# Performance work log

Measured on AMD Instinct MI355X. Metric: run time of the kernel, lower is better.

The kernel has to match this reference:

```python
import jax, jax.numpy as jnp
import numpy as np

N = 50000
E = 1600000
D_IN = 512
EPS = 1e-5


def setup_inputs() -> dict:
    key = jax.random.key(0)
    ks = jax.random.split(key, 20)
    p = lambda k, shape: jax.random.normal(k, shape, dtype=jnp.float32) * 0.05
    return {
        "x": jax.random.normal(ks[0], (N, D_IN), dtype=jnp.float32),
        "edge_index": jax.random.randint(ks[1], (2, E), 0, N),
        "edge_weight": jax.random.uniform(ks[2], (E,), dtype=jnp.float32),
        # conv1: ChebConv(512->400) with K=1,2,3 (weight per Chebyshev order)
        "W1a": p(ks[3], (1, D_IN, 400)), "b1a": p(ks[4], (400,)),
        "W1b": p(ks[5], (2, D_IN, 400)), "b1b": p(ks[6], (400,)),
        "W1c": p(ks[7], (3, D_IN, 400)), "b1c": p(ks[8], (400,)),
        "g1": jnp.ones((1200,), jnp.float32), "beta1": jnp.zeros((1200,), jnp.float32),
        # conv2: ChebConv(1200->100) with K=1,2,3
        "W2a": p(ks[9], (1, 1200, 100)), "b2a": p(ks[10], (100,)),
        "W2b": p(ks[11], (2, 1200, 100)), "b2b": p(ks[12], (100,)),
        "W2c": p(ks[13], (3, 1200, 100)), "b2c": p(ks[14], (100,)),
        "g2": jnp.ones((300,), jnp.float32), "beta2": jnp.zeros((300,), jnp.float32),
        "Wl": p(ks[15], (300, 10)), "bl": p(ks[16], (10,)),
    }


def _cheb(x, row, col, norm, W, b):
    """PyG ChebConv forward: out = sum_k T_k(L_hat) x @ W[k] + b.
    L_hat (sym norm, lambda_max=2) = -D^{-1/2} A D^{-1/2}, zero diagonal,
    applied as scatter: (L_hat h)[col] += norm_e * h[row]."""
    K = W.shape[0]
    n = x.shape[0]
    prop = lambda h: jax.ops.segment_sum(norm[:, None] * h[row], col, num_segments=n)
    out = x @ W[0]
    Tx_prev, Tx = x, None
    if K >= 2:
        Tx = prop(x)
        out = out + Tx @ W[1]
    for k in range(2, K):
        Tx_new = 2.0 * prop(Tx) - Tx_prev
        out = out + Tx_new @ W[k]
        Tx_prev, Tx = Tx, Tx_new
    return out + b


def _bn(h, g, beta):
    # BatchNorm over nodes (training-mode batch statistics, biased var)
    mu = h.mean(axis=0)
    var = h.var(axis=0)
    return (h - mu) * jax.lax.rsqrt(var + EPS) * g + beta


def reference(x, edge_index, edge_weight, W1a, b1a, W1b, b1b, W1c, b1c, g1, beta1,
              W2a, b2a, W2b, b2b, W2c, b2c, g2, beta2, Wl, bl):
    row, col = edge_index[0], edge_index[1]
    deg = jax.ops.segment_sum(edge_weight, row, num_segments=x.shape[0])
    safe = jnp.where(deg > 0, deg, 1.0)
    dis = jnp.where(deg > 0, jax.lax.rsqrt(safe), 0.0)  # deg^{-1/2}, inf -> 0
    norm = -dis[row] * edge_weight * dis[col]  # scaled-Laplacian edge weights

    h = jnp.concatenate([
        _cheb(x, row, col, norm, W1a, b1a),
        _cheb(x, row, col, norm, W1b, b1b),
        _cheb(x, row, col, norm, W1c, b1c)], axis=1)  # [N, 1200]
    h = jax.nn.relu(_bn(h, g1, beta1))

    h = jnp.concatenate([
        _cheb(h, row, col, norm, W2a, b2a),
        _cheb(h, row, col, norm, W2b, b2b),
        _cheb(h, row, col, norm, W2c, b2c)], axis=1)  # [N, 300]
    h = _bn(h, g2, beta2)

    logits = h @ Wl + bl  # [N, 10]
    return jax.nn.log_softmax(logits, axis=1)
```

## Files before the change

### kernel.cpp

```cpp
#include <hip/hip_runtime.h>
#include <math.h>

#define EPSB 1e-5f

typedef __attribute__((ext_vector_type(8))) short short8;
typedef __attribute__((ext_vector_type(4))) float floatx4;
typedef __attribute__((ext_vector_type(2))) float floatx2;

__device__ inline float bf2f(unsigned short h) {
  union { unsigned int u; float f; } v; v.u = ((unsigned int)h) << 16; return v.f;
}
__device__ inline unsigned short f2bf(float f) {
  union { float f; unsigned int u; } v; v.f = f;
  unsigned int r = v.u + 0x7fffu + ((v.u >> 16) & 1u);
  return (unsigned short)(r >> 16);
}

__device__ __forceinline__ void gl2lds16(const unsigned short* g, unsigned short* l) {
  __builtin_amdgcn_global_load_lds(
      (const __attribute__((address_space(1))) unsigned int*)g,
      (__attribute__((address_space(3))) unsigned int*)l, 16, 0, 0);
}

__device__ __forceinline__ void pk4(floatx2* a, uint4 g, floatx2 wv) {
  unsigned int u[4] = {g.x, g.y, g.z, g.w};
#pragma unroll
  for (int j = 0; j < 4; j++) {
    union { unsigned int q; float f; } lo, hi;
    lo.q = u[j] << 16;
    hi.q = u[j] & 0xffff0000u;
    floatx2 v; v[0] = lo.f; v[1] = hi.f;
    asm("v_pk_fma_f32 %0, %1, %2, %0" : "+v"(a[j]) : "v"(v), "v"(wv));
  }
}


__global__ void degcnt_kernel(const int* __restrict__ row, const int* __restrict__ col,
                              const float* __restrict__ ew,
                              float* __restrict__ deg, int* __restrict__ cnt, int E) {
  int e = blockIdx.x * blockDim.x + threadIdx.x;
  if (e < E) {
    atomicAdd(&deg[row[e]], ew[e]);
    atomicAdd(&cnt[col[e]], 1);
  }
}

__global__ void dis_kernel(float* deg, int n) {
  int i = blockIdx.x * blockDim.x + threadIdx.x;
  if (i < n) { float d = deg[i]; deg[i] = d > 0.f ? rsqrtf(d) : 0.f; }
}

__global__ __launch_bounds__(1024) void scan1_kernel(const int* __restrict__ cnt,
                                                     int* __restrict__ off,
                                                     int* __restrict__ bsum, int n) {
  __shared__ int buf[1024];
  int tid = threadIdx.x;
  int idx = blockIdx.x * 1024 + tid;
  int v = (idx < n) ? cnt[idx] : 0;
  buf[tid] = v;
  __syncthreads();
  for (int s = 1; s < 1024; s <<= 1) {
    int t = (tid >= s) ? buf[tid - s] : 0;
    __syncthreads();
    if (tid >= s) buf[tid] += t;
    __syncthreads();
  }
  if (idx < n) off[idx] = buf[tid] - v;
  if (tid == 1023) bsum[blockIdx.x] = buf[1023];
}

__global__ void scan2_kernel(int* __restrict__ bsum, int* __restrict__ off,
                             int nb, int n) {
  if (threadIdx.x == 0 && blockIdx.x == 0) {
    int run = 0;
    for (int k = 0; k < nb; k++) { int t = bsum[k]; bsum[k] = run; run += t; }
    off[n] = run;
  }
}

__global__ void scan3_kernel(int* __restrict__ off, const int* __restrict__ bsum, int n) {
  int i = blockIdx.x * blockDim.x + threadIdx.x;
  if (i < n) off[i] += bsum[i >> 10];
}

__global__ void copy_kernel(const int* __restrict__ src, int* __restrict__ dst, int n) {
  int i = blockIdx.x * blockDim.x + threadIdx.x;
  if (i < n) dst[i] = src[i];
}

__global__ void fill_kernel(const int* __restrict__ row, const int* __restrict__ col,
                            const float* __restrict__ ew, const float* __restrict__ dis,
                            int* __restrict__ wptr,
                            int2* __restrict__ ePack, int2* __restrict__ eA,
                            int2* __restrict__ eZ, int2* __restrict__ eU, int E) {
  int e = blockIdx.x * blockDim.x + threadIdx.x;
  if (e < E) {
    int r = row[e], c = col[e];
    int p = atomicAdd(&wptr[c], 1);
    float nv = -dis[r] * ew[e] * dis[c];
    int wb = __float_as_int(nv);
    ePack[p] = make_int2(r, wb);
    eA[p] = make_int2(r * 3072, wb);
    eZ[p] = make_int2(r * 608, wb);
    eU[p] = make_int2(r * 208, wb);
  }
}


__global__ void cast_x_kernel(const float* __restrict__ x, unsigned short* __restrict__ xb,
                              int N) {
  int idx = blockIdx.x * blockDim.x + threadIdx.x;
  if (idx >= N * 128) return;
  int row = idx >> 7, c4 = idx & 127;
  float4 v = *reinterpret_cast<const float4*>(x + (size_t)row * 512 + c4 * 4);
  union { unsigned int u[2]; } p;
  p.u[0] = (unsigned int)f2bf(v.x) | ((unsigned int)f2bf(v.y) << 16);
  p.u[1] = (unsigned int)f2bf(v.z) | ((unsigned int)f2bf(v.w) << 16);
  *reinterpret_cast<uint2*>(xb + (size_t)row * 1536 + c4 * 4) = make_uint2(p.u[0], p.u[1]);
}

__global__ void wprep_kernel(const float* __restrict__ W, unsigned short* __restrict__ Bt,
                             int Ktot, int Nout, int ldBt, int rowOff) {
  int idx = blockIdx.x * blockDim.x + threadIdx.x;
  if (idx >= Ktot * Nout) return;
  int k = idx / Nout, n = idx - k * Nout;
  Bt[(size_t)(rowOff + n) * ldBt + k] = f2bf(W[idx]);
}

__global__ void padzero_kernel(unsigned short* __restrict__ h, int N) {
  int i = blockIdx.x * blockDim.x + threadIdx.x;
  if (i >= N * 2) return;
  *reinterpret_cast<uint4*>(h + (size_t)(i >> 1) * 1216 + 1200 + (i & 1) * 8) =
      make_uint4(0, 0, 0, 0);
}

__global__ void bcat_kernel(const float* __restrict__ a, const float* __restrict__ b,
                            const float* __restrict__ c, float* __restrict__ dst) {
  int i = threadIdx.x;
  if (i < 100) dst[i] = a[i];
  else if (i < 200) dst[i] = b[i - 100];
  else if (i < 300) dst[i] = c[i - 200];
}

__global__ __launch_bounds__(256) void prop_chunk_kernel(
    unsigned short* __restrict__ base, int ld,
    int srcCol, int dstCol, int subCol,
    const int* __restrict__ off, const int2* __restrict__ eA,
    float scale, int N) {
  int chunk = blockIdx.x & 7;
  int g = blockIdx.x >> 3;
  int tid = threadIdx.x;
  int c8 = tid & 7;
  int v = g * 32 + (tid >> 3);
  bool valid = v < N;
  int vv = valid ? v : N - 1;
  int co = chunk * 64 + c8 * 8;
  const char* src = (const char*)(base + srcCol + co);
  int s = off[vv], e = off[vv + 1];
  floatx2 a2[4] = {}, b2[4] = {};
  int i = s;
  for (; i + 3 < e; i += 4) {
    int2 p0 = eA[i];
    int2 p1 = eA[i + 1];
    int2 p2 = eA[i + 2];
    int2 p3 = eA[i + 3];
    uint4 g0 = *reinterpret_cast<const uint4*>(src + (unsigned)p0.x);
    uint4 g1 = *reinterpret_cast<const uint4*>(src + (unsigned)p1.x);
    uint4 g2 = *reinterpret_cast<const uint4*>(src + (unsigned)p2.x);
    uint4 g3 = *reinterpret_cast<const uint4*>(src + (unsigned)p3.x);
    floatx2 w0; w0[0] = w0[1] = __int_as_float(p0.y);
    floatx2 w1; w1[0] = w1[1] = __int_as_float(p1.y);
    floatx2 w2; w2[0] = w2[1] = __int_as_float(p2.y);
    floatx2 w3; w3[0] = w3[1] = __int_as_float(p3.y);
    pk4(a2, g0, w0);
    pk4(b2, g1, w1);
    pk4(a2, g2, w2);
    pk4(b2, g3, w3);
  }
  for (; i < e; i++) {
    int2 p = eA[i];
    uint4 gg = *reinterpret_cast<const uint4*>(src + (unsigned)p.x);
    floatx2 wv; wv[0] = wv[1] = __int_as_float(p.y);
    pk4(a2, gg, wv);
  }
  if (!valid) return;
  float a[8];
#pragma unroll
  for (int j = 0; j < 4; j++) {
    a[2 * j]     = a2[j][0] + b2[j][0];
    a[2 * j + 1] = a2[j][1] + b2[j][1];
  }
  if (subCol >= 0) {
    uint4 sv = *reinterpret_cast<const uint4*>(base + subCol + co + (size_t)v * ld);
    a[0] = scale * a[0] - bf2f((unsigned short)(sv.x & 0xffff));
    a[1] = scale * a[1] - bf2f((unsigned short)(sv.x >> 16));
    a[2] = scale * a[2] - bf2f((unsigned short)(sv.y & 0xffff));
    a[3] = scale * a[3] - bf2f((unsigned short)(sv.y >> 16));
    a[4] = scale * a[4] - bf2f((unsigned short)(sv.z & 0xffff));
    a[5] = scale * a[5] - bf2f((unsigned short)(sv.z >> 16));
    a[6] = scale * a[6] - bf2f((unsigned short)(sv.w & 0xffff));
    a[7] = scale * a[7] - bf2f((unsigned short)(sv.w >> 16));
  }
  uint4 o;
  o.x = (unsigned int)f2bf(a[0]) | ((unsigned int)f2bf(a[1]) << 16);
  o.y = (unsigned int)f2bf(a[2]) | ((unsigned int)f2bf(a[3]) << 16);
  o.z = (unsigned int)f2bf(a[4]) | ((unsigned int)f2bf(a[5]) << 16);
  o.w = (unsigned int)f2bf(a[6]) | ((unsigned int)f2bf(a[7]) << 16);
  *reinterpret_cast<uint4*>(base + dstCol + co + (size_t)v * ld) = o;
}

__global__ void prop_z_kernel(const unsigned short* __restrict__ Zcat,
                              const int* __restrict__ off, const int2* __restrict__ eZ,
                              float* __restrict__ h2f, unsigned short* __restrict__ U1) {
  int v = blockIdx.x;
  int f8 = threadIdx.x;
  if (f8 >= 38) return;
  int s = off[v], e = off[v + 1];
  const char* srcB = (const char*)Zcat + f8 * 16;
  floatx2 a2[4] = {}, b2[4] = {};
  int i = s;
  for (; i + 3 < e; i += 4) {
    int2 p0 = eZ[i];
    int2 p1 = eZ[i + 1];
    int2 p2 = eZ[i + 2];
    int2 p3 = eZ[i + 3];
    uint4 g0 = *reinterpret_cast<const uint4*>(srcB + (unsigned)p0.x);
    uint4 g1 = *reinterpret_cast<const uint4*>(srcB + (unsigned)p1.x);
    uint4 g2 = *reinterpret_cast<const uint4*>(srcB + (unsigned)p2.x);
    uint4 g3 = *reinterpret_cast<const uint4*>(srcB + (unsigned)p3.x);
    floatx2 w0; w0[0] = w0[1] = __int_as_float(p0.y);
    floatx2 w1; w1[0] = w1[1] = __int_as_float(p1.y);
    floatx2 w2; w2[0] = w2[1] = __int_as_float(p2.y);
    floatx2 w3; w3[0] = w3[1] = __int_as_float(p3.y);
    pk4(a2, g0, w0);
    pk4(b2, g1, w1);
    pk4(a2, g2, w2);
    pk4(b2, g3, w3);
  }
  for (; i < e; i++) {
    int2 p = eZ[i];
    uint4 raw = *reinterpret_cast<const uint4*>(srcB + (unsigned)p.x);
    floatx2 wv; wv[0] = wv[1] = __int_as_float(p.y);
    pk4(a2, raw, wv);
  }
  float a[8];
#pragma unroll
  for (int j = 0; j < 4; j++) {
    a[2 * j]     = a2[j][0] + b2[j][0];
    a[2 * j + 1] = a2[j][1] + b2[j][1];
  }
  if (f8 < 25) {
    float* p = h2f + (size_t)v * 300 + 100 + f8 * 8;
#pragma unroll
    for (int j = 0; j < 8; j++) p[j] += a[j];
  } else {
    uint4 o;
    o.x = (unsigned int)f2bf(a[0]) | ((unsigned int)f2bf(a[1]) << 16);
    o.y = (unsigned int)f2bf(a[2]) | ((unsigned int)f2bf(a[3]) << 16);
    o.z = (unsigned int)f2bf(a[4]) | ((unsigned int)f2bf(a[5]) << 16);
    o.w = (unsigned int)f2bf(a[6]) | ((unsigned int)f2bf(a[7]) << 16);
    *reinterpret_cast<uint4*>(U1 + (size_t)v * 104 + (f8 - 25) * 8) = o;
  }
}

__global__ void prop_u_kernel(const unsigned short* __restrict__ U1,
                              const int* __restrict__ off, const int2* __restrict__ eU,
                              const unsigned short* __restrict__ Zcat,
                              float* __restrict__ h2f) {
  int v = blockIdx.x;
  int f8 = threadIdx.x;
  if (f8 >= 13) return;
  int s = off[v], e = off[v + 1];
  const char* srcB = (const char*)U1 + f8 * 16;
  floatx2 a2[4] = {}, b2[4] = {};
  int i = s;
  for (; i + 3 < e; i += 4) {
    int2 p0 = eU[i];
    int2 p1 = eU[i + 1];
    int2 p2 = eU[i + 2];
    int2 p3 = eU[i + 3];
    uint4 g0 = *reinterpret_cast<const uint4*>(srcB + (unsigned)p0.x);
    uint4 g1 = *reinterpret_cast<const uint4*>(srcB + (unsigned)p1.x);
    uint4 g2 = *reinterpret_cast<const uint4*>(srcB + (unsigned)p2.x);
    uint4 g3 = *reinterpret_cast<const uint4*>(srcB + (unsigned)p3.x);
    floatx2 w0; w0[0] = w0[1] = __int_as_float(p0.y);
    floatx2 w1; w1[0] = w1[1] = __int_as_float(p1.y);
    floatx2 w2; w2[0] = w2[1] = __int_as_float(p2.y);
    floatx2 w3; w3[0] = w3[1] = __int_as_float(p3.y);
    pk4(a2, g0, w0);
    pk4(b2, g1, w1);
    pk4(a2, g2, w2);
    pk4(b2, g3, w3);
  }
  for (; i < e; i++) {
    int2 p = eU[i];
    uint4 raw = *reinterpret_cast<const uint4*>(srcB + (unsigned)p.x);
    floatx2 wv; wv[0] = wv[1] = __int_as_float(p.y);
    pk4(a2, raw, wv);
  }
  float a[8];
#pragma unroll
  for (int j = 0; j < 4; j++) {
    a[2 * j]     = a2[j][0] + b2[j][0];
    a[2 * j + 1] = a2[j][1] + b2[j][1];
  }
  const unsigned short* z2 = Zcat + (size_t)v * 304 + 200;
  float* p = h2f + (size_t)v * 300 + 200;
#pragma unroll
  for (int j = 0; j < 8; j++) {
    int c = f8 * 8 + j;
    if (c < 100) p[c] += 2.f * a[j] - bf2f(z2[c]);
  }
}

__global__ __launch_bounds__(256) void gemm_bf16_kernel(
    const unsigned short* __restrict__ A, int lda,
    const unsigned short* __restrict__ Bt, int ldb,
    int M, int Nc, int K,
    const float* __restrict__ bias,
    unsigned short* __restrict__ Cb, float* __restrict__ Cf, int ldc, int c0,
    int accumulate) {
  __shared__ __align__(16) unsigned short As[128 * 32];
  __shared__ __align__(16) unsigned short Bs[128 * 32];
  int tid = threadIdx.x;
  int wave = tid >> 6, lane = tid & 63;
  int q = lane >> 4, mn = lane & 15;
  int wr = wave >> 1, wc = wave & 1;
  int row0 = blockIdx.y * 128, col0 = blockIdx.x * 128;
  floatx4 acc[4][4] = {};

  const unsigned short* ga[2];
  const unsigned short* gb[2];
  unsigned short* la[2];
  unsigned short* lb[2];
#pragma unroll
  for (int j = 0; j < 2; j++) {
    int c = j * 256 + tid;
    int r = c >> 2, cw = (c & 3) * 8;
    int gr = row0 + r; if (gr > M - 1) gr = M - 1;
    ga[j] = A + (size_t)gr * lda + cw;
    int gn = col0 + r; if (gn > Nc - 1) gn = Nc - 1;
    gb[j] = Bt + (size_t)gn * ldb + cw;
    la[j] = &As[(j * 256 + wave * 64) * 8];
    lb[j] = &Bs[(j * 256 + wave * 64) * 8];
  }

  for (int k0 = 0; k0 < K; k0 += 32) {
#pragma unroll
    for (int j = 0; j < 2; j++) {
      gl2lds16(ga[j] + k0, la[j]);
      gl2lds16(gb[j] + k0, lb[j]);
    }
    __syncthreads();

    short8 af[4], bf[4];
#pragma unroll
    for (int i = 0; i < 4; i++) {
      af[i] = *reinterpret_cast<const short8*>(&As[(wr * 64 + i * 16 + mn) * 32 + q * 8]);
      bf[i] = *reinterpret_cast<const short8*>(&Bs[(wc * 64 + i * 16 + mn) * 32 + q * 8]);
    }
#pragma unroll
    for (int mi = 0; mi < 4; mi++)
#pragma unroll
      for (int ni = 0; ni < 4; ni++)
        acc[mi][ni] = __builtin_amdgcn_mfma_f32_16x16x32_bf16(af[mi], bf[ni], acc[mi][ni], 0, 0, 0);
    __syncthreads();
  }

#pragma unroll
  for (int mi = 0; mi < 4; mi++) {
#pragma unroll
    for (int ni = 0; ni < 4; ni++) {
      int gcol = col0 + wc * 64 + ni * 16 + mn;
      if (gcol >= Nc) continue;
      float b = bias ? bias[gcol] : 0.f;
#pragma unroll
      for (int r = 0; r < 4; r++) {
        int grow = row0 + wr * 64 + mi * 16 + q * 4 + r;
        if (grow >= M) continue;
        float v = acc[mi][ni][r] + b;
        if (Cb) {
          Cb[(size_t)grow * ldc + c0 + gcol] = f2bf(v);
        } else {
          float* p = Cf + (size_t)grow * ldc + c0 + gcol;
          if (accumulate) v += *p;
          *p = v;
        }
      }
    }
  }
}

__global__ void bn_stats_bf16_kernel(const unsigned short* __restrict__ h, int ld, int C,
                                     int N, float* __restrict__ sums) {
  int c = blockIdx.x * blockDim.x + threadIdx.x;
  if (c >= C) return;
  int r0 = blockIdx.y * 256;
  int r1 = min(N, r0 + 256);
  float s = 0.f, s2 = 0.f;
  for (int r = r0; r < r1; r++) {
    float v = bf2f(h[(size_t)r * ld + c]);
    s += v; s2 += v * v;
  }
  atomicAdd(&sums[c], s);
  atomicAdd(&sums[C + c], s2);
}

__global__ void scsh_kernel(const float* __restrict__ sums, const float* __restrict__ g,
                            const float* __restrict__ beta, float invN, int C,
                            float* __restrict__ scSh) {
  int c = blockIdx.x * blockDim.x + threadIdx.x;
  if (c >= C) return;
  float mu = sums[c] * invN;
  float var = sums[C + c] * invN - mu * mu;
  float s = rsqrtf(var + EPSB) * g[c];
  scSh[c] = s;
  scSh[C + c] = beta[c] - mu * s;
}

__global__ void bn_apply_bf16_kernel(unsigned short* __restrict__ h, int ld, int C8, int N,
                                     const float* __restrict__ scSh, int Cfull, int relu) {
  int idx = blockIdx.x * blockDim.x + threadIdx.x;
  if (idx >= N * C8) return;
  int row = idx / C8, c8 = idx - row * C8;
  unsigned short* p = h + (size_t)row * ld + c8 * 8;
  uint4 raw = *reinterpret_cast<uint4*>(p);
  float v[8];
  v[0] = bf2f((unsigned short)(raw.x & 0xffff)); v[1] = bf2f((unsigned short)(raw.x >> 16));
  v[2] = bf2f((unsigned short)(raw.y & 0xffff)); v[3] = bf2f((unsigned short)(raw.y >> 16));
  v[4] = bf2f((unsigned short)(raw.z & 0xffff)); v[5] = bf2f((unsigned short)(raw.z >> 16));
  v[6] = bf2f((unsigned short)(raw.w & 0xffff)); v[7] = bf2f((unsigned short)(raw.w >> 16));
#pragma unroll
  for (int j = 0; j < 8; j++) {
    int c = c8 * 8 + j;
    float o = v[j] * scSh[c] + scSh[Cfull + c];
    if (relu) o = fmaxf(o, 0.f);
    v[j] = o;
  }
  uint4 o;
  o.x = (unsigned int)f2bf(v[0]) | ((unsigned int)f2bf(v[1]) << 16);
  o.y = (unsigned int)f2bf(v[2]) | ((unsigned int)f2bf(v[3]) << 16);
  o.z = (unsigned int)f2bf(v[4]) | ((unsigned int)f2bf(v[5]) << 16);
  o.w = (unsigned int)f2bf(v[6]) | ((unsigned int)f2bf(v[7]) << 16);
  *reinterpret_cast<uint4*>(p) = o;
}

__global__ void bn_stats_kernel(const float* __restrict__ h, int C, int N,
                                float* __restrict__ sums) {
  int c = blockIdx.x * blockDim.x + threadIdx.x;
  if (c >= C) return;
  int r0 = blockIdx.y * 256;
  int r1 = min(N, r0 + 256);
  float s = 0.f, s2 = 0.f;
  for (int r = r0; r < r1; r++) {
    float v = h[(size_t)r * C + c];
    s += v; s2 += v * v;
  }
  atomicAdd(&sums[c], s);
  atomicAdd(&sums[C + c], s2);
}

__global__ void bn_apply_kernel(float* __restrict__ h, int C, int N,
                                const float* __restrict__ sums, const float* __restrict__ g,
                                const float* __restrict__ beta, float invN, int relu) {
  int C4 = C >> 2;
  int c4 = blockIdx.x * blockDim.x + threadIdx.x;
  if (c4 >= C4) return;
  float sc[4], sh[4];
#pragma unroll
  for (int j = 0; j < 4; j++) {
    int c = c4 * 4 + j;
    float mu = sums[c] * invN;
    float var = sums[C + c] * invN - mu * mu;
    float s = rsqrtf(var + EPSB) * g[c];
    sc[j] = s; sh[j] = beta[c] - mu * s;
  }
  int r0 = blockIdx.y * 256, r1 = min(N, r0 + 256);
  for (int r = r0; r < r1; r++) {
    float4* p = reinterpret_cast<float4*>(h + (size_t)r * C) + c4;
    float4 v = *p;
    v.x = v.x * sc[0] + sh[0]; v.y = v.y * sc[1] + sh[1];
    v.z = v.z * sc[2] + sh[2]; v.w = v.w * sc[3] + sh[3];
    if (relu) {
      v.x = fmaxf(v.x, 0.f); v.y = fmaxf(v.y, 0.f);
      v.z = fmaxf(v.z, 0.f); v.w = fmaxf(v.w, 0.f);
    }
    *p = v;
  }
}


__global__ __launch_bounds__(256) void final_bn_kernel(const float* __restrict__ h2,
                                                       const float* __restrict__ scSh,
                                                       const float* __restrict__ Wl,
                                                       const float* __restrict__ bl,
                                                       float* __restrict__ out, int N) {
  __shared__ float Ws[3000];
  __shared__ float S[600];
  for (int i = threadIdx.x; i < 3000; i += 256) Ws[i] = Wl[i];
  for (int i = threadIdx.x; i < 600; i += 256) S[i] = scSh[i];
  __syncthreads();
  int r = blockIdx.x * blockDim.x + threadIdx.x;
  if (r >= N) return;
  float acc[10];
#pragma unroll
  for (int c = 0; c < 10; c++) acc[c] = bl[c];
  const float* hr = h2 + (size_t)r * 300;
  for (int k = 0; k < 300; k++) {
    float x = hr[k] * S[k] + S[300 + k];
#pragma unroll
    for (int c = 0; c < 10; c++) acc[c] += x * Ws[k * 10 + c];
  }
  float mx = acc[0];
#pragma unroll
  for (int c = 1; c < 10; c++) mx = fmaxf(mx, acc[c]);
  float se = 0.f;
#pragma unroll
  for (int c = 0; c < 10; c++) se += expf(acc[c] - mx);
  float lz = mx + logf(se);
#pragma unroll
  for (int c = 0; c < 10; c++) out[(size_t)r * 10 + c] = acc[c] - lz;
}

__global__ __launch_bounds__(256) void final_kernel(const float* __restrict__ h2,
                                                    const float* __restrict__ Wl,
                                                    const float* __restrict__ bl,
                                                    float* __restrict__ out, int N) {
  __shared__ float Ws[3000];
  for (int i = threadIdx.x; i < 3000; i += 256) Ws[i] = Wl[i];
  __syncthreads();
  int r = blockIdx.x * blockDim.x + threadIdx.x;
  if (r >= N) return;
  float acc[10];
#pragma unroll
  for (int c = 0; c < 10; c++) acc[c] = bl[c];
  const float* hr = h2 + (size_t)r * 300;
  for (int k = 0; k < 300; k++) {
    float x = hr[k];
#pragma unroll
    for (int c = 0; c < 10; c++) acc[c] += x * Ws[k * 10 + c];
  }
  float mx = acc[0];
#pragma unroll
  for (int c = 1; c < 10; c++) mx = fmaxf(mx, acc[c]);
  float se = 0.f;
#pragma unroll
  for (int c = 0; c < 10; c++) se += expf(acc[c] - mx);
  float lz = mx + logf(se);
#pragma unroll
  for (int c = 0; c < 10; c++) out[(size_t)r * 10 + c] = acc[c] - lz;
}


__global__ void prop_kernel(const float* __restrict__ src, int srcLd4, int D4,
                            const int* __restrict__ off, const int2* __restrict__ ePack,
                            float* __restrict__ dst, int dstLd4,
                            const float* __restrict__ sub, int subLd4, float scale) {
  int v = blockIdx.x;
  int f4 = threadIdx.x;
  if (f4 >= D4) return;
  int s = off[v], e = off[v + 1];
  float ax = 0.f, ay = 0.f, az = 0.f, aw = 0.f;
  for (int i = s; i < e; i++) {
    int2 p = ePack[i];
    float w = __int_as_float(p.y);
    const float4 hv = *reinterpret_cast<const float4*>(src + ((size_t)p.x * srcLd4 + f4) * 4);
    ax += w * hv.x; ay += w * hv.y; az += w * hv.z; aw += w * hv.w;
  }
  float4 o;
  if (sub) {
    const float4 sv = *reinterpret_cast<const float4*>(sub + ((size_t)v * subLd4 + f4) * 4);
    o.x = scale * ax - sv.x; o.y = scale * ay - sv.y;
    o.z = scale * az - sv.z; o.w = scale * aw - sv.w;
  } else {
    o.x = ax; o.y = ay; o.z = az; o.w = aw;
  }
  *reinterpret_cast<float4*>(dst + ((size_t)v * dstLd4 + f4) * 4) = o;
}

#define BM 64
#define BN 64
#define BK 16

__global__ __launch_bounds__(256) void gemm_kernel(
    const float* __restrict__ A, int lda,
    const float* __restrict__ B, int ldb,
    float* __restrict__ C, int ldc, int c0,
    int M, int Nc, int K,
    const float* __restrict__ bias, int accumulate) {
  __shared__ float As[BK][BM + 4];
  __shared__ float Bs[BK][BN + 4];
  int tid = threadIdx.x;
  int tx = tid & 15, ty = tid >> 4;
  int row0 = blockIdx.y * BM, col0 = blockIdx.x * BN;
  float acc[4][4] = {};
  int aM = tid >> 2;
  int aK = (tid & 3) << 2;
  int bK = tid >> 4;
  int bN = (tid & 15) << 2;
  for (int k0 = 0; k0 < K; k0 += BK) {
    float4 av = make_float4(0.f, 0.f, 0.f, 0.f);
    int ar = row0 + aM;
    if (ar < M && k0 + aK < K)
      av = *reinterpret_cast<const float4*>(A + (size_t)ar * lda + k0 + aK);
    As[aK + 0][aM] = av.x; As[aK + 1][aM] = av.y;
    As[aK + 2][aM] = av.z; As[aK + 3][aM] = av.w;
    float4 bv = make_float4(0.f, 0.f, 0.f, 0.f);
    int bc = col0 + bN;
    if (bc < Nc && k0 + bK < K)
      bv = *reinterpret_cast<const float4*>(B + (size_t)(k0 + bK) * ldb + bc);
    Bs[bK][bN + 0] = bv.x; Bs[bK][bN + 1] = bv.y;
    Bs[bK][bN + 2] = bv.z; Bs[bK][bN + 3] = bv.w;
    __syncthreads();
#pragma unroll
    for (int k = 0; k < BK; k++) {
      float a0 = As[k][ty * 4 + 0], a1 = As[k][ty * 4 + 1];
      float a2 = As[k][ty * 4 + 2], a3 = As[k][ty * 4 + 3];
      float b0 = Bs[k][tx * 4 + 0], b1 = Bs[k][tx * 4 + 1];
      float b2 = Bs[k][tx * 4 + 2], b3 = Bs[k][tx * 4 + 3];
      acc[0][0] += a0 * b0; acc[0][1] += a0 * b1; acc[0][2] += a0 * b2; acc[0][3] += a0 * b3;
      acc[1][0] += a1 * b0; acc[1][1] += a1 * b1; acc[1][2] += a1 * b2; acc[1][3] += a1 * b3;
      acc[2][0] += a2 * b0; acc[2][1] += a2 * b1; acc[2][2] += a2 * b2; acc[2][3] += a2 * b3;
      acc[3][0] += a3 * b0; acc[3][1] += a3 * b1; acc[3][2] += a3 * b2; acc[3][3] += a3 * b3;
    }
    __syncthreads();
  }
#pragma unroll
  for (int i = 0; i < 4; i++) {
    int r = row0 + ty * 4 + i;
    if (r >= M) continue;
#pragma unroll
    for (int j = 0; j < 4; j++) {
      int c = col0 + tx * 4 + j;
      if (c >= Nc) continue;
      float v = acc[i][j];
      if (bias) v += bias[c];
      float* p = C + (size_t)r * ldc + c0 + c;
      if (accumulate) *p += v; else *p = v;
    }
  }
}


extern "C" void kernel_launch(void* const* d_in, const int* in_sizes, int n_in,
                              void* d_out, int out_size, void* d_ws, size_t ws_size,
                              hipStream_t stream) {
  const float* x   = (const float*)d_in[0];
  const int*   ei  = (const int*)d_in[1];
  const float* ew  = (const float*)d_in[2];
  const float* W1a = (const float*)d_in[3];
  const float* b1a = (const float*)d_in[4];
  const float* W1b = (const float*)d_in[5];
  const float* b1b = (const float*)d_in[6];
  const float* W1c = (const float*)d_in[7];
  const float* b1c = (const float*)d_in[8];
  const float* g1  = (const float*)d_in[9];
  const float* be1 = (const float*)d_in[10];
  const float* W2a = (const float*)d_in[11];
  const float* b2a = (const float*)d_in[12];
  const float* W2b = (const float*)d_in[13];
  const float* b2b = (const float*)d_in[14];
  const float* W2c = (const float*)d_in[15];
  const float* b2c = (const float*)d_in[16];
  const float* g2  = (const float*)d_in[17];
  const float* be2 = (const float*)d_in[18];
  const float* Wl  = (const float*)d_in[19];
  const float* bl  = (const float*)d_in[20];
  float* out = (float*)d_out;

  const int N = in_sizes[0] / 512;
  const int E = in_sizes[1] / 2;
  const int* row = ei;
  const int* col = ei + E;
  (void)n_in; (void)out_size;

  int eb = (E + 255) / 256;
  int nb = (N + 255) / 256;
  int nb1 = (N + 1023) / 1024;

  char* ws = (char*)d_ws;
  size_t o = 0;
  int2*  ePack = (int2*)(ws + o);  o += (size_t)E * 8;
  int2*  eA    = (int2*)(ws + o);  o += (size_t)E * 8;
  int2*  eZ    = (int2*)(ws + o);  o += (size_t)E * 8;
  int2*  eU    = (int2*)(ws + o);  o += (size_t)E * 8;
  float* dis   = (float*)(ws + o); o += (size_t)N * 4;
  int*   cnt   = (int*)(ws + o);   o += (size_t)N * 4;
  int*   off   = (int*)(ws + o);   o += (size_t)(N + 4) * 4;
  int*   wptr  = (int*)(ws + o);   o += (size_t)N * 4;
  int*   bsum  = (int*)(ws + o);   o += (size_t)(nb1 + 4) * 4;
  float* sums  = (float*)(ws + o); o += 2400 * 4;
  float* scSh  = (float*)(ws + o); o += 2400 * 4;
  float* bcat  = (float*)(ws + o); o += 304 * 4;
  o = (o + 255) & ~(size_t)255;
  size_t oCommon = o;

  size_t oA = oCommon;
  unsigned short* Bt1a = (unsigned short*)(ws + oA); oA += (size_t)400 * 512 * 2;
  unsigned short* Bt1b = (unsigned short*)(ws + oA); oA += (size_t)400 * 1024 * 2;
  unsigned short* Bt1c = (unsigned short*)(ws + oA); oA += (size_t)400 * 1536 * 2;
  unsigned short* Bt2cat0 = (unsigned short*)(ws + oA); oA += (size_t)304 * 1216 * 2;
  unsigned short* Bt2z    = (unsigned short*)(ws + oA); oA += (size_t)304 * 1216 * 2;
  oA = (oA + 255) & ~(size_t)255;
  unsigned short* h1n = (unsigned short*)(ws + oA); oA += (size_t)N * 1216 * 2;
  oA = (oA + 255) & ~(size_t)255;
  float* h2f = (float*)(ws + oA); oA += (size_t)N * 300 * 4;
  oA = (oA + 255) & ~(size_t)255;
  unsigned short* Xcat = (unsigned short*)(ws + oA); oA += (size_t)N * 1536 * 2;
  unsigned short* Zcat = Xcat;
  unsigned short* U1 = Xcat + (size_t)N * 304;

  bool planA = (ws_size >= oA);

  hipMemsetAsync(dis, 0, (size_t)N * 4, stream);
  hipMemsetAsync(cnt, 0, (size_t)N * 4, stream);
  degcnt_kernel<<<eb, 256, 0, stream>>>(row, col, ew, dis, cnt, E);
  dis_kernel<<<nb, 256, 0, stream>>>(dis, N);
  scan1_kernel<<<nb1, 1024, 0, stream>>>(cnt, off, bsum, N);
  scan2_kernel<<<1, 64, 0, stream>>>(bsum, off, nb1, N);
  scan3_kernel<<<nb, 256, 0, stream>>>(off, bsum, N);
  copy_kernel<<<nb, 256, 0, stream>>>(off, wptr, N);
  fill_kernel<<<eb, 256, 0, stream>>>(row, col, ew, dis, wptr, ePack, eA, eZ, eU, E);

  if (planA) {
    wprep_kernel<<<(400 * 512 + 255) / 256, 256, 0, stream>>>(W1a, Bt1a, 512, 400, 512, 0);
    wprep_kernel<<<(400 * 1024 + 255) / 256, 256, 0, stream>>>(W1b, Bt1b, 1024, 400, 1024, 0);
    wprep_kernel<<<(400 * 1536 + 255) / 256, 256, 0, stream>>>(W1c, Bt1c, 1536, 400, 1536, 0);
    hipMemsetAsync(Bt2cat0, 0, (size_t)304 * 1216 * 2, stream);
    hipMemsetAsync(Bt2z, 0, (size_t)304 * 1216 * 2, stream);
    wprep_kernel<<<(100 * 1200 + 255) / 256, 256, 0, stream>>>(W2a, Bt2cat0, 1200, 100, 1216, 0);
    wprep_kernel<<<(100 * 1200 + 255) / 256, 256, 0, stream>>>(W2b, Bt2cat0, 1200, 100, 1216, 100);
    wprep_kernel<<<(100 * 1200 + 255) / 256, 256, 0, stream>>>(W2c, Bt2cat0, 1200, 100, 1216, 200);
    wprep_kernel<<<(100 * 1200 + 255) / 256, 256, 0, stream>>>(W2b + 1200 * 100, Bt2z, 1200, 100, 1216, 0);
    wprep_kernel<<<(100 * 1200 + 255) / 256, 256, 0, stream>>>(W2c + 1200 * 100, Bt2z, 1200, 100, 1216, 100);
    wprep_kernel<<<(100 * 1200 + 255) / 256, 256, 0, stream>>>(W2c + 2 * 1200 * 100, Bt2z, 1200, 100, 1216, 200);
    bcat_kernel<<<1, 320, 0, stream>>>(b2a, b2b, b2c, bcat);
    cast_x_kernel<<<(N * 128 + 255) / 256, 256, 0, stream>>>(x, Xcat, N);
    padzero_kernel<<<(N * 2 + 255) / 256, 256, 0, stream>>>(h1n, N);

    int gridP = ((N + 31) / 32) * 8;
    prop_chunk_kernel<<<gridP, 256, 0, stream>>>(Xcat, 1536, 0, 512, -1,
                                                 off, eA, 1.f, N);
    prop_chunk_kernel<<<gridP, 256, 0, stream>>>(Xcat, 1536, 512, 1024, 0,
                                                 off, eA, 2.f, N);

    dim3 gA((400 + 127) / 128, (N + 127) / 128);
    gemm_bf16_kernel<<<gA, 256, 0, stream>>>(Xcat, 1536, Bt1a, 512, N, 400, 512,
                                             b1a, h1n, nullptr, 1216, 0, 0);
    gemm_bf16_kernel<<<gA, 256, 0, stream>>>(Xcat, 1536, Bt1b, 1024, N, 400, 1024,
                                             b1b, h1n, nullptr, 1216, 400, 0);
    gemm_bf16_kernel<<<gA, 256, 0, stream>>>(Xcat, 1536, Bt1c, 1536, N, 400, 1536,
                                             b1c, h1n, nullptr, 1216, 800, 0);

    hipMemsetAsync(sums, 0, 2400 * 4, stream);
    dim3 s1g((1200 + 255) / 256, (N + 255) / 256);
    bn_stats_bf16_kernel<<<s1g, 256, 0, stream>>>(h1n, 1216, 1200, N, sums);
    scsh_kernel<<<(1200 + 255) / 256, 256, 0, stream>>>(sums, g1, be1, 1.f / (float)N, 1200, scSh);
    bn_apply_bf16_kernel<<<((size_t)N * 150 + 255) / 256, 256, 0, stream>>>(
        h1n, 1216, 150, N, scSh, 1200, 1);

    dim3 gB0((300 + 127) / 128, (N + 127) / 128);
    gemm_bf16_kernel<<<gB0, 256, 0, stream>>>(h1n, 1216, Bt2cat0, 1216, N, 300, 1216,
                                              bcat, nullptr, h2f, 300, 0, 0);

    dim3 gBz((304 + 127) / 128, (N + 127) / 128);
    gemm_bf16_kernel<<<gBz, 256, 0, stream>>>(h1n, 1216, Bt2z, 1216, N, 304, 1216,
                                              nullptr, Zcat, nullptr, 304, 0, 0);

    prop_z_kernel<<<N, 64, 0, stream>>>(Zcat, off, eZ, h2f, U1);
    prop_u_kernel<<<N, 64, 0, stream>>>(U1, off, eU, Zcat, h2f);

    hipMemsetAsync(sums, 0, 2400 * 4, stream);
    dim3 s2g((300 + 255) / 256, (N + 255) / 256);
    bn_stats_kernel<<<s2g, 256, 0, stream>>>(h2f, 300, N, sums);
    scsh_kernel<<<(300 + 255) / 256, 256, 0, stream>>>(sums, g2, be2, 1.f / (float)N, 300, scSh);
    final_bn_kernel<<<nb, 256, 0, stream>>>(h2f, scSh, Wl, bl, out, N);
    return;
  }

  size_t oB = oCommon;
  float* h2 = (float*)(ws + oB); oB += (size_t)N * 300 * 4;
  oB = (oB + 255) & ~(size_t)255;
  float* h1 = (float*)(ws + oB); oB += (size_t)N * 1200 * 4;
  oB = (oB + 255) & ~(size_t)255;
  size_t avail = (ws_size > oB) ? (ws_size - oB) : 0;
  int C1 = 64;
  { const int opts[4] = {512, 256, 128, 64};
    for (int i = 0; i < 4; i++)
      if ((size_t)2 * N * opts[i] * 4 <= avail) { C1 = opts[i]; break; } }
  int C2 = 100;
  { const int opts[6] = {1200, 600, 400, 300, 200, 100};
    for (int i = 0; i < 6; i++)
      if ((size_t)2 * N * opts[i] * 4 <= avail) { C2 = opts[i]; break; } }
  int maxC = C1 > C2 ? C1 : C2;
  float* S1 = (float*)(ws + oB);
  float* S2 = S1 + (size_t)N * maxC;

  dim3 g1d((400 + BN - 1) / BN, (N + BM - 1) / BM);
  gemm_kernel<<<g1d, 256, 0, stream>>>(x, 512, W1a, 400, h1, 1200, 0,   N, 400, 512, b1a, 0);
  gemm_kernel<<<g1d, 256, 0, stream>>>(x, 512, W1b, 400, h1, 1200, 400, N, 400, 512, b1b, 0);
  gemm_kernel<<<g1d, 256, 0, stream>>>(x, 512, W1c, 400, h1, 1200, 800, N, 400, 512, b1c, 0);
  for (int c = 0; c < 512; c += C1) {
    int D4 = C1 / 4;
    int bt = ((D4 + 63) / 64) * 64;
    prop_kernel<<<N, bt, 0, stream>>>(x + c, 128, D4, off, ePack, S1, D4, nullptr, 0, 1.f);
    gemm_kernel<<<g1d, 256, 0, stream>>>(S1, C1, W1b + (size_t)(512 + c) * 400, 400, h1, 1200, 400, N, 400, C1, nullptr, 1);
    gemm_kernel<<<g1d, 256, 0, stream>>>(S1, C1, W1c + (size_t)(512 + c) * 400, 400, h1, 1200, 800, N, 400, C1, nullptr, 1);
    prop_kernel<<<N, bt, 0, stream>>>(S1, D4, D4, off, ePack, S2, D4, x + c, 128, 2.f);
    gemm_kernel<<<g1d, 256, 0, stream>>>(S2, C1, W1c + (size_t)(2 * 512 + c) * 400, 400, h1, 1200, 800, N, 400, C1, nullptr, 1);
  }

  hipMemsetAsync(sums, 0, 2400 * 4, stream);
  dim3 s1g((1200 + 255) / 256, (N + 255) / 256);
  bn_stats_kernel<<<s1g, 256, 0, stream>>>(h1, 1200, N, sums);
  dim3 a1g((300 + 63) / 64, (N + 255) / 256);
  bn_apply_kernel<<<a1g, 64, 0, stream>>>(h1, 1200, N, sums, g1, be1, 1.f / (float)N, 1);

  dim3 g2d((100 + BN - 1) / BN, (N + BM - 1) / BM);
  gemm_kernel<<<g2d, 256, 0, stream>>>(h1, 1200, W2a, 100, h2, 300, 0,   N, 100, 1200, b2a, 0);
  gemm_kernel<<<g2d, 256, 0, stream>>>(h1, 1200, W2b, 100, h2, 300, 100, N, 100, 1200, b2b, 0);
  gemm_kernel<<<g2d, 256, 0, stream>>>(h1, 1200, W2c, 100, h2, 300, 200, N, 100, 1200, b2c, 0);
  for (int c = 0; c < 1200; c += C2) {
    int D4 = C2 / 4;
    int bt = ((D4 + 63) / 64) * 64;
    prop_kernel<<<N, bt, 0, stream>>>(h1 + c, 300, D4, off, ePack, S1, D4, nullptr, 0, 1.f);
    gemm_kernel<<<g2d, 256, 0, stream>>>(S1, C2, W2b + (size_t)(1200 + c) * 100, 100, h2, 300, 100, N, 100, C2, nullptr, 1);
    gemm_kernel<<<g2d, 256, 0, stream>>>(S1, C2, W2c + (size_t)(1200 + c) * 100, 100, h2, 300, 200, N, 100, C2, nullptr, 1);
    prop_kernel<<<N, bt, 0, stream>>>(S1, D4, D4, off, ePack, S2, D4, h1 + c, 300, 2.f);
    gemm_kernel<<<g2d, 256, 0, stream>>>(S2, C2, W2c + (size_t)(2 * 1200 + c) * 100, 100, h2, 300, 200, N, 100, C2, nullptr, 1);
  }

  hipMemsetAsync(sums, 0, 2400 * 4, stream);
  dim3 s2g((300 + 255) / 256, (N + 255) / 256);
  bn_stats_kernel<<<s2g, 256, 0, stream>>>(h2, 300, N, sums);
  dim3 a2g((75 + 63) / 64, (N + 255) / 256);
  bn_apply_kernel<<<a2g, 64, 0, stream>>>(h2, 300, N, sums, g2, be2, 1.f / (float)N, 0);

  final_kernel<<<nb, 256, 0, stream>>>(h2, Wl, bl, out, N);
}
```

Measured before the change: 1.919 ms.

## Share one CSR edge array and retile sparse propagation kernels for locality

Drops the three per-stride pre-multiplied edge arrays and computes row offsets with shifts from the single packed edge list, which removes 3×E×8 bytes of writes in fill. The layer-1 propagation now processes 32-column chunks over 64 nodes, with blocks grouped by column half. The layer-2 prop_z and prop_u kernels change from one block per node to many nodes per block split into column chunks. Zcat and U1 row strides are padded to 320 and 128 elements so offsets reduce to shift arithmetic, at the cost of more gather passes over the edge list per column chunk.

```diff
diff --git a/kernel.cpp b/kernel.cpp
--- a/kernel.cpp
+++ b/kernel.cpp
@@ -90,19 +90,13 @@
 
 __global__ void fill_kernel(const int* __restrict__ row, const int* __restrict__ col,
                             const float* __restrict__ ew, const float* __restrict__ dis,
-                            int* __restrict__ wptr,
-                            int2* __restrict__ ePack, int2* __restrict__ eA,
-                            int2* __restrict__ eZ, int2* __restrict__ eU, int E) {
+                            int* __restrict__ wptr, int2* __restrict__ ePack, int E) {
   int e = blockIdx.x * blockDim.x + threadIdx.x;
   if (e < E) {
     int r = row[e], c = col[e];
     int p = atomicAdd(&wptr[c], 1);
     float nv = -dis[r] * ew[e] * dis[c];
-    int wb = __float_as_int(nv);
-    ePack[p] = make_int2(r, wb);
-    eA[p] = make_int2(r * 3072, wb);
-    eZ[p] = make_int2(r * 608, wb);
-    eU[p] = make_int2(r * 208, wb);
+    ePack[p] = make_int2(r, __float_as_int(nv));
   }
 }
 
@@ -143,31 +137,38 @@
 }
 
 __global__ __launch_bounds__(256) void prop_chunk_kernel(
-    unsigned short* __restrict__ base, int ld,
+    unsigned short* __restrict__ base,
     int srcCol, int dstCol, int subCol,
-    const int* __restrict__ off, const int2* __restrict__ eA,
+    const int* __restrict__ off, const int2* __restrict__ eP,
     float scale, int N) {
-  int chunk = blockIdx.x & 7;
-  int g = blockIdx.x >> 3;
+  int ng8 = gridDim.x >> 1;
+  int half = (blockIdx.x >= ng8) ? 1 : 0;
+  int q = blockIdx.x - half * ng8;
+  int colchunk = half * 8 + (q & 7);
+  int g = q >> 3;
   int tid = threadIdx.x;
-  int c8 = tid & 7;
-  int v = g * 32 + (tid >> 3);
+  int c4 = tid & 3;
+  int v = g * 64 + (tid >> 2);
   bool valid = v < N;
   int vv = valid ? v : N - 1;
-  int co = chunk * 64 + c8 * 8;
+  int co = colchunk * 32 + c4 * 8;
   const char* src = (const char*)(base + srcCol + co);
   int s = off[vv], e = off[vv + 1];
   floatx2 a2[4] = {}, b2[4] = {};
   int i = s;
   for (; i + 3 < e; i += 4) {
-    int2 p0 = eA[i];
-    int2 p1 = eA[i + 1];
-    int2 p2 = eA[i + 2];
-    int2 p3 = eA[i + 3];
-    uint4 g0 = *reinterpret_cast<const uint4*>(src + (unsigned)p0.x);
-    uint4 g1 = *reinterpret_cast<const uint4*>(src + (unsigned)p1.x);
-    uint4 g2 = *reinterpret_cast<const uint4*>(src + (unsigned)p2.x);
-    uint4 g3 = *reinterpret_cast<const uint4*>(src + (unsigned)p3.x);
+    int2 p0 = eP[i];
+    int2 p1 = eP[i + 1];
+    int2 p2 = eP[i + 2];
+    int2 p3 = eP[i + 3];
+    unsigned o0 = ((unsigned)p0.x << 11) + ((unsigned)p0.x << 10);
+    unsigned o1 = ((unsigned)p1.x << 11) + ((unsigned)p1.x << 10);
+    unsigned o2 = ((unsigned)p2.x << 11) + ((unsigned)p2.x << 10);
+    unsigned o3 = ((unsigned)p3.x << 11) + ((unsigned)p3.x << 10);
+    uint4 g0 = *reinterpret_cast<const uint4*>(src + o0);
+    uint4 g1 = *reinterpret_cast<const uint4*>(src + o1);
+    uint4 g2 = *reinterpret_cast<const uint4*>(src + o2);
+    uint4 g3 = *reinterpret_cast<const uint4*>(src + o3);
     floatx2 w0; w0[0] = w0[1] = __int_as_float(p0.y);
     floatx2 w1; w1[0] = w1[1] = __int_as_float(p1.y);
     floatx2 w2; w2[0] = w2[1] = __int_as_float(p2.y);
@@ -178,8 +179,9 @@
     pk4(b2, g3, w3);
   }
   for (; i < e; i++) {
-    int2 p = eA[i];
-    uint4 gg = *reinterpret_cast<const uint4*>(src + (unsigned)p.x);
+    int2 p = eP[i];
+    unsigned o0 = ((unsigned)p.x << 11) + ((unsigned)p.x << 10);
+    uint4 gg = *reinterpret_cast<const uint4*>(src + o0);
     floatx2 wv; wv[0] = wv[1] = __int_as_float(p.y);
     pk4(a2, gg, wv);
   }
@@ -191,7 +193,7 @@
     a[2 * j + 1] = a2[j][1] + b2[j][1];
   }
   if (subCol >= 0) {
-    uint4 sv = *reinterpret_cast<const uint4*>(base + subCol + co + (size_t)v * ld);
+    uint4 sv = *reinterpret_cast<const uint4*>(base + subCol + co + (size_t)v * 1536);
     a[0] = scale * a[0] - bf2f((unsigned short)(sv.x & 0xffff));
     a[1] = scale * a[1] - bf2f((unsigned short)(sv.x >> 16));
     a[2] = scale * a[2] - bf2f((unsigned short)(sv.y & 0xffff));
@@ -206,28 +208,38 @@
   o.y = (unsigned int)f2bf(a[2]) | ((unsigned int)f2bf(a[3]) << 16);
   o.z = (unsigned int)f2bf(a[4]) | ((unsigned int)f2bf(a[5]) << 16);
   o.w = (unsigned int)f2bf(a[6]) | ((unsigned int)f2bf(a[7]) << 16);
-  *reinterpret_cast<uint4*>(base + dstCol + co + (size_t)v * ld) = o;
-}
-
-__global__ void prop_z_kernel(const unsigned short* __restrict__ Zcat,
-                              const int* __restrict__ off, const int2* __restrict__ eZ,
-                              float* __restrict__ h2f, unsigned short* __restrict__ U1) {
-  int v = blockIdx.x;
-  int f8 = threadIdx.x;
-  if (f8 >= 38) return;
+  *reinterpret_cast<uint4*>(base + dstCol + co + (size_t)v * 1536) = o;
+}
+
+__global__ __launch_bounds__(320) void prop_z_kernel(
+    const unsigned short* __restrict__ Zcat,
+    const int* __restrict__ off, const int2* __restrict__ eP,
+    float* __restrict__ h2f, unsigned short* __restrict__ U1, int N) {
+  int chunk = blockIdx.x & 7;
+  int g = blockIdx.x >> 3;
+  int tid = threadIdx.x;
+  int node = tid / 5;
+  int lane = tid - node * 5;
+  int v = g * 64 + node;
+  int unit = chunk * 5 + lane;
+  if (v >= N || unit >= 38) return;
   int s = off[v], e = off[v + 1];
-  const char* srcB = (const char*)Zcat + f8 * 16;
+  const char* srcB = (const char*)Zcat + unit * 16;
   floatx2 a2[4] = {}, b2[4] = {};
   int i = s;
   for (; i + 3 < e; i += 4) {
-    int2 p0 = eZ[i];
-    int2 p1 = eZ[i + 1];
-    int2 p2 = eZ[i + 2];
-    int2 p3 = eZ[i + 3];
-    uint4 g0 = *reinterpret_cast<const uint4*>(srcB + (unsigned)p0.x);
-    uint4 g1 = *reinterpret_cast<const uint4*>(srcB + (unsigned)p1.x);
-    uint4 g2 = *reinterpret_cast<const uint4*>(srcB + (unsigned)p2.x);
-    uint4 g3 = *reinterpret_cast<const uint4*>(srcB + (unsigned)p3.x);
+    int2 p0 = eP[i];
+    int2 p1 = eP[i + 1];
+    int2 p2 = eP[i + 2];
+    int2 p3 = eP[i + 3];
+    unsigned o0 = ((unsigned)p0.x << 9) + ((unsigned)p0.x << 7);
+    unsigned o1 = ((unsigned)p1.x << 9) + ((unsigned)p1.x << 7);
+    unsigned o2 = ((unsigned)p2.x << 9) + ((unsigned)p2.x << 7);
+    unsigned o3 = ((unsigned)p3.x << 9) + ((unsigned)p3.x << 7);
+    uint4 g0 = *reinterpret_cast<const uint4*>(srcB + o0);
+    uint4 g1 = *reinterpret_cast<const uint4*>(srcB + o1);
+    uint4 g2 = *reinterpret_cast<const uint4*>(srcB + o2);
+    uint4 g3 = *reinterpret_cast<const uint4*>(srcB + o3);
     floatx2 w0; w0[0] = w0[1] = __int_as_float(p0.y);
     floatx2 w1; w1[0] = w1[1] = __int_as_float(p1.y);
     floatx2 w2; w2[0] = w2[1] = __int_as_float(p2.y);
@@ -238,8 +250,9 @@
     pk4(b2, g3, w3);
   }
   for (; i < e; i++) {
-    int2 p = eZ[i];
-    uint4 raw = *reinterpret_cast<const uint4*>(srcB + (unsigned)p.x);
+    int2 p = eP[i];
+    unsigned o0 = ((unsigned)p.x << 9) + ((unsigned)p.x << 7);
+    uint4 raw = *reinterpret_cast<const uint4*>(srcB + o0);
     floatx2 wv; wv[0] = wv[1] = __int_as_float(p.y);
     pk4(a2, raw, wv);
   }
@@ -249,8 +262,8 @@
     a[2 * j]     = a2[j][0] + b2[j][0];
     a[2 * j + 1] = a2[j][1] + b2[j][1];
   }
-  if (f8 < 25) {
-    float* p = h2f + (size_t)v * 300 + 100 + f8 * 8;
+  if (unit < 25) {
+    float* p = h2f + (size_t)v * 300 + 100 + unit * 8;
 #pragma unroll
     for (int j = 0; j < 8; j++) p[j] += a[j];
   } else {
@@ -259,30 +272,37 @@
     o.y = (unsigned int)f2bf(a[2]) | ((unsigned int)f2bf(a[3]) << 16);
     o.z = (unsigned int)f2bf(a[4]) | ((unsigned int)f2bf(a[5]) << 16);
     o.w = (unsigned int)f2bf(a[6]) | ((unsigned int)f2bf(a[7]) << 16);
-    *reinterpret_cast<uint4*>(U1 + (size_t)v * 104 + (f8 - 25) * 8) = o;
-  }
-}
-
-__global__ void prop_u_kernel(const unsigned short* __restrict__ U1,
-                              const int* __restrict__ off, const int2* __restrict__ eU,
-                              const unsigned short* __restrict__ Zcat,
-                              float* __restrict__ h2f) {
-  int v = blockIdx.x;
-  int f8 = threadIdx.x;
-  if (f8 >= 13) return;
+    *reinterpret_cast<uint4*>(U1 + (size_t)v * 128 + (unit - 25) * 8) = o;
+  }
+}
+
+__global__ __launch_bounds__(256) void prop_u_kernel(
+    const unsigned short* __restrict__ U1,
+    const int* __restrict__ off, const int2* __restrict__ eP,
+    const unsigned short* __restrict__ Zcat, float* __restrict__ h2f, int N) {
+  int chunk = blockIdx.x & 7;
+  int g = blockIdx.x >> 3;
+  int tid = threadIdx.x;
+  int v = g * 128 + (tid >> 1);
+  int unit = chunk * 2 + (tid & 1);
+  if (v >= N || unit >= 13) return;
   int s = off[v], e = off[v + 1];
-  const char* srcB = (const char*)U1 + f8 * 16;
+  const char* srcB = (const char*)U1 + unit * 16;
   floatx2 a2[4] = {}, b2[4] = {};
   int i = s;
   for (; i + 3 < e; i += 4) {
-    int2 p0 = eU[i];
-    int2 p1 = eU[i + 1];
-    int2 p2 = eU[i + 2];
-    int2 p3 = eU[i + 3];
-    uint4 g0 = *reinterpret_cast<const uint4*>(srcB + (unsigned)p0.x);
-    uint4 g1 = *reinterpret_cast<const uint4*>(srcB + (unsigned)p1.x);
-    uint4 g2 = *reinterpret_cast<const uint4*>(srcB + (unsigned)p2.x);
-    uint4 g3 = *reinterpret_cast<const uint4*>(srcB + (unsigned)p3.x);
+    int2 p0 = eP[i];
+    int2 p1 = eP[i + 1];
+    int2 p2 = eP[i + 2];
+    int2 p3 = eP[i + 3];
+    unsigned o0 = (unsigned)p0.x << 8;
+    unsigned o1 = (unsigned)p1.x << 8;
+    unsigned o2 = (unsigned)p2.x << 8;
+    unsigned o3 = (unsigned)p3.x << 8;
+    uint4 g0 = *reinterpret_cast<const uint4*>(srcB + o0);
+    uint4 g1 = *reinterpret_cast<const uint4*>(srcB + o1);
+    uint4 g2 = *reinterpret_cast<const uint4*>(srcB + o2);
+    uint4 g3 = *reinterpret_cast<const uint4*>(srcB + o3);
     floatx2 w0; w0[0] = w0[1] = __int_as_float(p0.y);
     floatx2 w1; w1[0] = w1[1] = __int_as_float(p1.y);
     floatx2 w2; w2[0] = w2[1] = __int_as_float(p2.y);
@@ -293,8 +313,9 @@
     pk4(b2, g3, w3);
   }
   for (; i < e; i++) {
-    int2 p = eU[i];
-    uint4 raw = *reinterpret_cast<const uint4*>(srcB + (unsigned)p.x);
+    int2 p = eP[i];
+    unsigned o0 = (unsigned)p.x << 8;
+    uint4 raw = *reinterpret_cast<const uint4*>(srcB + o0);
     floatx2 wv; wv[0] = wv[1] = __int_as_float(p.y);
     pk4(a2, raw, wv);
   }
@@ -304,11 +325,11 @@
     a[2 * j]     = a2[j][0] + b2[j][0];
     a[2 * j + 1] = a2[j][1] + b2[j][1];
   }
-  const unsigned short* z2 = Zcat + (size_t)v * 304 + 200;
+  const unsigned short* z2 = Zcat + (size_t)v * 320 + 200;
   float* p = h2f + (size_t)v * 300 + 200;
 #pragma unroll
   for (int j = 0; j < 8; j++) {
-    int c = f8 * 8 + j;
+    int c = unit * 8 + j;
     if (c < 100) p[c] += 2.f * a[j] - bf2f(z2[c]);
   }
 }
@@ -681,9 +702,6 @@
   char* ws = (char*)d_ws;
   size_t o = 0;
   int2*  ePack = (int2*)(ws + o);  o += (size_t)E * 8;
-  int2*  eA    = (int2*)(ws + o);  o += (size_t)E * 8;
-  int2*  eZ    = (int2*)(ws + o);  o += (size_t)E * 8;
-  int2*  eU    = (int2*)(ws + o);  o += (size_t)E * 8;
   float* dis   = (float*)(ws + o); o += (size_t)N * 4;
   int*   cnt   = (int*)(ws + o);   o += (size_t)N * 4;
   int*   off   = (int*)(ws + o);   o += (size_t)(N + 4) * 4;
@@ -708,7 +726,7 @@
   oA = (oA + 255) & ~(size_t)255;
   unsigned short* Xcat = (unsigned short*)(ws + oA); oA += (size_t)N * 1536 * 2;
   unsigned short* Zcat = Xcat;
-  unsigned short* U1 = Xcat + (size_t)N * 304;
+  unsigned short* U1 = Xcat + (size_t)N * 320;
 
   bool planA = (ws_size >= oA);
 
@@ -720,7 +738,7 @@
   scan2_kernel<<<1, 64, 0, stream>>>(bsum, off, nb1, N);
   scan3_kernel<<<nb, 256, 0, stream>>>(off, bsum, N);
   copy_kernel<<<nb, 256, 0, stream>>>(off, wptr, N);
-  fill_kernel<<<eb, 256, 0, stream>>>(row, col, ew, dis, wptr, ePack, eA, eZ, eU, E);
+  fill_kernel<<<eb, 256, 0, stream>>>(row, col, ew, dis, wptr, ePack, E);
 
   if (planA) {
     wprep_kernel<<<(400 * 512 + 255) / 256, 256, 0, stream>>>(W1a, Bt1a, 512, 400, 512, 0);
@@ -738,11 +756,9 @@
     cast_x_kernel<<<(N * 128 + 255) / 256, 256, 0, stream>>>(x, Xcat, N);
     padzero_kernel<<<(N * 2 + 255) / 256, 256, 0, stream>>>(h1n, N);
 
-    int gridP = ((N + 31) / 32) * 8;
-    prop_chunk_kernel<<<gridP, 256, 0, stream>>>(Xcat, 1536, 0, 512, -1,
-                                                 off, eA, 1.f, N);
-    prop_chunk_kernel<<<gridP, 256, 0, stream>>>(Xcat, 1536, 512, 1024, 0,
-                                                 off, eA, 2.f, N);
+    int ng64 = (N + 63) / 64;
+    prop_chunk_kernel<<<ng64 * 16, 256, 0, stream>>>(Xcat, 0, 512, -1, off, ePack, 1.f, N);
+    prop_chunk_kernel<<<ng64 * 16, 256, 0, stream>>>(Xcat, 512, 1024, 0, off, ePack, 2.f, N);
 
     dim3 gA((400 + 127) / 128, (N + 127) / 128);
     gemm_bf16_kernel<<<gA, 256, 0, stream>>>(Xcat, 1536, Bt1a, 512, N, 400, 512,
@@ -765,10 +781,11 @@
 
     dim3 gBz((304 + 127) / 128, (N + 127) / 128);
     gemm_bf16_kernel<<<gBz, 256, 0, stream>>>(h1n, 1216, Bt2z, 1216, N, 304, 1216,
-                                              nullptr, Zcat, nullptr, 304, 0, 0);
-
-    prop_z_kernel<<<N, 64, 0, stream>>>(Zcat, off, eZ, h2f, U1);
-    prop_u_kernel<<<N, 64, 0, stream>>>(U1, off, eU, Zcat, h2f);
+                                              nullptr, Zcat, nullptr, 320, 0, 0);
+
+    prop_z_kernel<<<ng64 * 8, 320, 0, stream>>>(Zcat, off, ePack, h2f, U1, N);
+    int ng128 = (N + 127) / 128;
+    prop_u_kernel<<<ng128 * 8, 256, 0, stream>>>(U1, off, ePack, Zcat, h2f, N);
 
     hipMemsetAsync(sums, 0, 2400 * 4, stream);
     dim3 s2g((300 + 255) / 256, (N + 255) / 256);
```

Result: slower. 2.715 ms (+41.5%).
